# Kernel tuning notes

Hardware: AMD Instinct MI355X
Metric: run time of the kernel (lower is better)

## Reference

```python
import jax, jax.numpy as jnp
import numpy as np

HID, NH, HD = 1024, 16, 64
B, S = 2, 2048


def _gammas(nh):
    # gammas = 1 - exp(linspace(log(1/512), log(1/32), nh))
    lin = np.linspace(np.log(1.0 / 512.0), np.log(1.0 / 32.0), nh)
    return jnp.asarray(1.0 - np.exp(lin), dtype=jnp.float32)


def setup_inputs() -> dict:
    key = jax.random.key(0)
    ks = jax.random.split(key, 6)
    x = jax.random.normal(ks[0], (B, S, HID), dtype=jnp.float32)
    # Per-head retention projection weights (Retention has its own q/k/v of [head_size, head_size])
    wq = jax.random.normal(ks[1], (NH, HD, HD), dtype=jnp.float32) / HD
    wk = jax.random.normal(ks[2], (NH, HD, HD), dtype=jnp.float32) / HD
    wv = jax.random.normal(ks[3], (NH, HD, HD), dtype=jnp.float32) / HD
    w1 = jax.random.normal(ks[4], (HID, HID), dtype=jnp.float32) / HID
    w2 = jax.random.normal(ks[5], (HID, HID), dtype=jnp.float32) / HID
    gn_scale = jnp.ones((HID,), dtype=jnp.float32)
    gn_bias = jnp.zeros((HID,), dtype=jnp.float32)
    return {"x": x, "wq": wq, "wk": wk, "wv": wv, "w1": w1, "w2": w2,
            "gn_scale": gn_scale, "gn_bias": gn_bias}


def reference(x, wq, wk, wv, w1, w2, gn_scale, gn_bias):
    b, s, h = x.shape
    nh, hd = wq.shape[0], wq.shape[1]
    gammas = _gammas(nh)  # [nh]

    xh = x.reshape(b, s, nh, hd)
    q = jnp.einsum('bsnd,nde->bsne', xh, wq)
    k = jnp.einsum('bsnd,nde->bsne', xh, wk)
    v = jnp.einsum('bsnd,nde->bsne', xh, wv)

    # causal decay mask D[n, s, t] = gamma_n ** (s - t) for s >= t else 0
    idx = jnp.arange(s)
    diff = (idx[:, None] - idx[None, :]).astype(jnp.float32)  # [s, s]
    safe = jnp.maximum(diff, 0.0)
    D = jnp.where(diff >= 0,
                  jnp.exp(safe[None] * jnp.log(gammas)[:, None, None]),
                  0.0)  # [nh, s, s]

    scores = jnp.einsum('bsnd,btnd->bnst', q, k) * D[None]      # [b, nh, s, s]
    ret = jnp.einsum('bnst,btnd->bsnd', scores, v)              # [b, s, nh, hd]

    # GroupNorm(num_groups=nh, num_channels=h) over flattened [b*s, h]:
    # normalize within each head-group of hd channels, affine per-channel, eps=1e-5
    mean = ret.mean(axis=-1, keepdims=True)
    var = ret.var(axis=-1, keepdims=True)
    norm = (ret - mean) / jnp.sqrt(var + 1e-5)
    norm = norm.reshape(b, s, h) * gn_scale + gn_bias

    gate = jnp.matmul(x, w1)
    out = gate * jax.nn.sigmoid(gate) + norm  # swish-gated branch + retention
    return jnp.matmul(out, w2)
```

## Files before the change

kernel.cpp:

```cpp
#include <hip/hip_runtime.h>

#define HIDD 1024
#define NHH  16
#define HDD  64
#define BBB  2
#define SSS  2048
#define BS   (BBB * SSS)

typedef __attribute__((ext_vector_type(8))) _Float16 half8;
typedef __attribute__((ext_vector_type(4))) _Float16 half4;
typedef __attribute__((ext_vector_type(4))) float    f32x4;

#define LSCALE 2048.0f
#define LINV   (1.0f / 2048.0f)

static __device__ __forceinline__ f32x4 mfma16h(half8 a, half8 b, f32x4 c) {
    return __builtin_amdgcn_mfma_f32_16x16x32_f16(a, b, c, 0, 0, 0);
}

static __device__ __forceinline__ void split2h(float v, _Float16& h, _Float16& l) {
    h = (_Float16)v;
    l = (_Float16)((v - (float)h) * LSCALE);
}

static __device__ __forceinline__ void gl_lds16(const _Float16* g, _Float16* l) {
    __builtin_amdgcn_global_load_lds(
        (const __attribute__((address_space(1))) unsigned int*)g,
        (__attribute__((address_space(3))) unsigned int*)l,
        16, 0, 0);
}

__global__ __launch_bounds__(256) void k_wprep(const float* __restrict__ wq,
                                               const float* __restrict__ wk,
                                               const float* __restrict__ wv,
                                               _Float16* __restrict__ WTh,
                                               _Float16* __restrict__ WTl) {
    const int blk = blockIdx.x;
    const int mat = blk >> 4, n = blk & 15;
    const float* src = (mat == 0 ? wq : mat == 1 ? wk : wv) + (size_t)n * 4096;
    for (int c = threadIdx.x; c < 4096; c += 256) {
        int e = c >> 6, d = c & 63;
        float v = src[d * 64 + e];
        _Float16 h, l;
        split2h(v, h, l);
        WTh[(size_t)blk * 4096 + c] = h;
        WTl[(size_t)blk * 4096 + c] = l;
    }
}

__global__ __launch_bounds__(512) void k_proj_mfma(const float* __restrict__ x,
                                                   const _Float16* __restrict__ WTh,
                                                   const _Float16* __restrict__ WTl,
                                                   _Float16* __restrict__ Qh, _Float16* __restrict__ Ql,
                                                   _Float16* __restrict__ Kh, _Float16* __restrict__ Kl,
                                                   _Float16* __restrict__ VTh, _Float16* __restrict__ VTl) {
    const int n  = blockIdx.y;
    const int R0 = blockIdx.x * 128;
    const int tid = threadIdx.x;
    const int w = tid >> 6, lane = tid & 63;
    const int hi = lane >> 4, lo = lane & 15;

    __shared__ __align__(16) _Float16 smem[27648];

    half8 ah[2], al[2];
#pragma unroll
    for (int kf = 0; kf < 2; kf++) {
        const float* xp = x + (size_t)(R0 + 16 * w + lo) * HIDD + n * HDD + kf * 32 + 8 * hi;
        float4 v0 = *(const float4*)xp;
        float4 v1 = *(const float4*)(xp + 4);
        float vv[8] = { v0.x, v0.y, v0.z, v0.w, v1.x, v1.y, v1.z, v1.w };
#pragma unroll
        for (int j = 0; j < 8; ++j) {
            _Float16 h, l;
            split2h(vv[j], h, l);
            ah[kf][j] = h; al[kf][j] = l;
        }
    }

    for (int c = tid; c < 3072; c += 512) {
        int m = c >> 10, rest = c & 1023, hl = rest >> 9, cc = rest & 511;
        int r = cc >> 3, j8 = (cc & 7) << 3;
        const _Float16* src = (hl ? WTl : WTh) + ((size_t)(m * NHH + n)) * 4096 + r * 64 + j8;
        *(half8*)&smem[(m * 2 + hl) * 4608 + r * 72 + j8] = *(const half8*)src;
    }
    __syncthreads();

    const int bq = R0 >> 11;
    const int sr = R0 & 2047;
    const size_t bn = (size_t)(bq * NHH + n);
    float vkeep[4][4][2];

    for (int mat = 0; mat < 3; ++mat) {
        const _Float16* bh_base = smem + (mat * 2 + 0) * 4608;
        const _Float16* bl_base = smem + (mat * 2 + 1) * 4608;
        f32x4 a0[4], a1[4];
#pragma unroll
        for (int eb = 0; eb < 4; ++eb) {
            a0[eb] = (f32x4){0.f, 0.f, 0.f, 0.f};
            a1[eb] = (f32x4){0.f, 0.f, 0.f, 0.f};
        }
#pragma unroll
        for (int eb = 0; eb < 4; ++eb) {
            half8 bh0 = *(const half8*)&bh_base[(16 * eb + lo) * 72 + 8 * hi];
            half8 bh1 = *(const half8*)&bh_base[(16 * eb + lo) * 72 + 32 + 8 * hi];
            half8 bl0 = *(const half8*)&bl_base[(16 * eb + lo) * 72 + 8 * hi];
            half8 bl1 = *(const half8*)&bl_base[(16 * eb + lo) * 72 + 32 + 8 * hi];
            a0[eb] = mfma16h(ah[0], bh0, a0[eb]);
            a0[eb] = mfma16h(ah[1], bh1, a0[eb]);
            a1[eb] = mfma16h(ah[0], bl0, a1[eb]);
            a1[eb] = mfma16h(al[0], bh0, a1[eb]);
            a1[eb] = mfma16h(ah[1], bl1, a1[eb]);
            a1[eb] = mfma16h(al[1], bh1, a1[eb]);
        }

        if (mat < 2) {
            _Float16* Dh = (mat == 0) ? Qh : Kh;
            _Float16* Dl = (mat == 0) ? Ql : Kl;
#pragma unroll
            for (int eb = 0; eb < 4; ++eb)
#pragma unroll
                for (int r = 0; r < 4; ++r) {
                    int gr = R0 + 16 * w + 4 * hi + r;
                    int s = gr & 2047;
                    float val = a0[eb][r] + a1[eb][r] * LINV;
                    _Float16 h, l;
                    split2h(val, h, l);
                    size_t idx = (bn * SSS + s) * HDD + 16 * eb + lo;
                    Dh[idx] = h; Dl[idx] = l;
                }
        } else {
#pragma unroll
            for (int eb = 0; eb < 4; ++eb)
#pragma unroll
                for (int r = 0; r < 4; ++r) {
                    vkeep[eb][r][0] = a0[eb][r];
                    vkeep[eb][r][1] = a1[eb][r];
                }
        }
    }

    __syncthreads();
    _Float16* tbh = smem;
    _Float16* tbl = smem + 8704;
#pragma unroll
    for (int eb = 0; eb < 4; ++eb)
#pragma unroll
        for (int r = 0; r < 4; ++r) {
            int rl = 16 * w + 4 * hi + r;
            int ch = 16 * eb + lo;
            _Float16 h, l;
            split2h(vkeep[eb][r][0] + vkeep[eb][r][1] * LINV, h, l);
            tbh[ch * 136 + rl] = h;
            tbl[ch * 136 + rl] = l;
        }
    __syncthreads();
    for (int c = tid; c < 1024; c += 512) {
        int ch = c >> 4, s8 = (c & 15) << 3;
        int a64 = s8 & 64;
        int s0 = s8 & 63;
        int basePerm = a64 + (s0 & 32) + ((s0 >> 3) & 3) * 4;
        const _Float16* th = &tbh[ch * 136];
        const _Float16* tl = &tbl[ch * 136];
        half4 h0 = *(const half4*)(th + basePerm);
        half4 h1 = *(const half4*)(th + basePerm + 16);
        half4 l0 = *(const half4*)(tl + basePerm);
        half4 l1 = *(const half4*)(tl + basePerm + 16);
        half8 oh = {h0[0], h0[1], h0[2], h0[3], h1[0], h1[1], h1[2], h1[3]};
        half8 ol = {l0[0], l0[1], l0[2], l0[3], l1[0], l1[1], l1[2], l1[3]};
        size_t gi = (bn * HDD + ch) * SSS + sr + s8;
        *(half8*)(VTh + gi) = oh;
        *(half8*)(VTl + gi) = ol;
    }
}

__global__ __launch_bounds__(256) void k_ret_mfma(const _Float16* __restrict__ Qh, const _Float16* __restrict__ Ql,
                                                  const _Float16* __restrict__ Kh, const _Float16* __restrict__ Kl,
                                                  const _Float16* __restrict__ VTh, const _Float16* __restrict__ VTl,
                                                  const float* __restrict__ gns,
                                                  const float* __restrict__ gnb,
                                                  float* __restrict__ normb) {
    const int n = blockIdx.y, b = blockIdx.z;
    const int qt = (n < 8) ? ((int)gridDim.x - 1 - (int)blockIdx.x) : (int)blockIdx.x;
    const int tid = threadIdx.x;
    const int w = tid >> 6, lane = tid & 63;
    const int hi = lane >> 4, lo = lane & 15;

    const double l512 = -6.2383246250395075;
    const double l32  = -3.4657359027997265;
    double lin = l512 + (double)n * (l32 - l512) / 15.0;
    float gamma = (float)(1.0 - exp(lin));
    float l2g = log2f(gamma);
    int dmax = (int)(16.0f / (-l2g)) + 1;

    const int qb = qt * 64;
    const int qw = qb + 16 * w;
    int stb_start = (qb > dmax) ? ((qb - dmax) >> 5) : 0;
    const int stb_end  = 2 * qt + 1;
    const int stb_diag = qw >> 5;

    const size_t bn = (size_t)(b * NHH + n);
    const _Float16* Qhp = Qh + bn * SSS * HDD;
    const _Float16* Qlp = Ql + bn * SSS * HDD;
    const _Float16* Khp = Kh + bn * SSS * HDD;
    const _Float16* Klp = Kl + bn * SSS * HDD;
    const _Float16* Vhp = VTh + bn * HDD * SSS;
    const _Float16* Vlp = VTl + bn * HDD * SSS;

    half8 qfh[2], qfl[2];
#pragma unroll
    for (int kf = 0; kf < 2; kf++) {
        size_t o = (size_t)(qw + lo) * HDD + kf * 32 + 8 * hi;
        qfh[kf] = *(const half8*)(Qhp + o);
        qfl[kf] = *(const half8*)(Qlp + o);
    }

    f32x4 acc0[4], acc1[4];
#pragma unroll
    for (int e = 0; e < 4; e++) {
        acc0[e] = (f32x4){0.f, 0.f, 0.f, 0.f};
        acc1[e] = (f32x4){0.f, 0.f, 0.f, 0.f};
    }

    __shared__ __align__(16) _Float16 ksh[4096];
    __shared__ __align__(16) _Float16 ksl[4096];
    __shared__ __align__(16) _Float16 vsh[4096];
    __shared__ __align__(16) _Float16 vsl[4096];

    const _Float16* sg = (w == 0) ? Khp : (w == 1) ? Klp : (w == 2) ? Vhp : Vlp;
    _Float16* slds = (w == 0) ? ksh : (w == 1) ? ksl : (w == 2) ? vsh : vsl;
    size_t goff;
    if (w < 2) goff = (size_t)(lane >> 3) * HDD + (size_t)((((lane & 7) ^ ((lane >> 3) & 7))) << 3);
    else       goff = (size_t)(lane >> 2) * SSS + (size_t)((((lane & 3) ^ ((lane >> 3) & 3))) << 3);

    auto issue = [&](int tbase, int pb) {
        _Float16* Lb = slds + pb * 2048;
        if (w < 2) {
#pragma unroll
            for (int i = 0; i < 4; ++i)
                gl_lds16(sg + (size_t)(tbase + 8 * i) * HDD + goff, Lb + i * 512);
        } else {
#pragma unroll
            for (int i = 0; i < 4; ++i)
                gl_lds16(sg + (size_t)(16 * i) * SSS + tbase + goff, Lb + i * 512);
        }
    };

    const int ks0 = ((hi ^ (lo & 7)) << 3);
    const int ks1 = (((4 + hi) ^ (lo & 7)) << 3);
    const int vs0 = ((hi ^ ((lo >> 1) & 3)) << 3);

    float ftile = exp2f((float)(qw + lo - stb_start * 32) * l2g);
    const float gi16   = exp2f(-16.0f * l2g);
    const float ginv32 = exp2f(-32.0f * l2g);
    float f4[4];
#pragma unroll
    for (int r = 0; r < 4; ++r) f4[r] = exp2f(-(float)(4 * hi + r) * l2g);

    int pb = 0;
    issue(stb_start * 32, 0);
    __syncthreads();

    for (int stb = stb_start; stb <= stb_end; ++stb) {
        const int tbase = stb * 32;
        if (stb < stb_end) issue(tbase + 32, pb ^ 1);

        const bool active = (tbase <= qw + 15) && (tbase + 31 >= qw - dmax);
        if (active) {
            const bool dm = (stb == stb_diag);
            const _Float16* kh_ = &ksh[pb * 2048];
            const _Float16* kl_ = &ksl[pb * 2048];
            const _Float16* vh_ = &vsh[pb * 2048];
            const _Float16* vl_ = &vsl[pb * 2048];
            _Float16 ph4[2][4], pl4[2][4];
#pragma unroll
            for (int tt = 0; tt < 2; ++tt) {
                int rb = (16 * tt + lo) * 64;
                half8 kh0 = *(const half8*)&kh_[rb + ks0];
                half8 kh1 = *(const half8*)&kh_[rb + ks1];
                half8 kl0 = *(const half8*)&kl_[rb + ks0];
                half8 kl1 = *(const half8*)&kl_[rb + ks1];
                f32x4 s0 = (f32x4){0.f, 0.f, 0.f, 0.f};
                f32x4 s1 = (f32x4){0.f, 0.f, 0.f, 0.f};
                s0 = mfma16h(kh0, qfh[0], s0);
                s0 = mfma16h(kh1, qfh[1], s0);
                s1 = mfma16h(kl0, qfh[0], s1);
                s1 = mfma16h(kh0, qfl[0], s1);
                s1 = mfma16h(kl1, qfh[1], s1);
                s1 = mfma16h(kh1, qfl[1], s1);
                const float g = tt ? ftile * gi16 : ftile;
#pragma unroll
                for (int r = 0; r < 4; r++) {
                    float p = (s0[r] + s1[r] * LINV) * (g * f4[r]);
                    if (dm) {
                        int diff = (qw + lo) - (tbase + 16 * tt + 4 * hi + r);
                        if (diff < 0) p = 0.0f;
                    }
                    split2h(p, ph4[tt][r], pl4[tt][r]);
                }
            }
            half8 pfh = (half8){ph4[0][0], ph4[0][1], ph4[0][2], ph4[0][3],
                                ph4[1][0], ph4[1][1], ph4[1][2], ph4[1][3]};
            half8 pfl = (half8){pl4[0][0], pl4[0][1], pl4[0][2], pl4[0][3],
                                pl4[1][0], pl4[1][1], pl4[1][2], pl4[1][3]};
#pragma unroll
            for (int e = 0; e < 4; e++) {
                int vb = (16 * e + lo) * 32 + vs0;
                half8 vh0 = *(const half8*)&vh_[vb];
                half8 vl0 = *(const half8*)&vl_[vb];
                acc0[e] = mfma16h(pfh, vh0, acc0[e]);
                acc1[e] = mfma16h(pfh, vl0, acc1[e]);
                acc1[e] = mfma16h(pfl, vh0, acc1[e]);
            }
        }
        ftile *= ginv32;
        __syncthreads();
        pb ^= 1;
    }

    f32x4 accf[4];
#pragma unroll
    for (int e = 0; e < 4; e++)
#pragma unroll
        for (int r = 0; r < 4; r++)
            accf[e][r] = acc0[e][r] + acc1[e][r] * LINV;

    float s[4], sq[4];
#pragma unroll
    for (int r = 0; r < 4; r++) {
        s[r] = 0.f; sq[r] = 0.f;
#pragma unroll
        for (int e = 0; e < 4; e++) { float v = accf[e][r]; s[r] += v; sq[r] += v * v; }
    }
#pragma unroll
    for (int mask = 1; mask < 16; mask <<= 1)
#pragma unroll
        for (int r = 0; r < 4; r++) {
            s[r]  += __shfl_xor(s[r],  mask);
            sq[r] += __shfl_xor(sq[r], mask);
        }
#pragma unroll
    for (int e = 0; e < 4; e++)
#pragma unroll
        for (int r = 0; r < 4; r++) {
            float mean = s[r] * (1.0f / 64.0f);
            float var  = sq[r] * (1.0f / 64.0f) - mean * mean;
            float rstd = rsqrtf(var + 1e-5f);
            int ch = 16 * e + lo;
            int sg2 = qw + 4 * hi + r;
            float nv = (accf[e][r] - mean) * rstd;
            nv = nv * gns[n * 64 + ch] + gnb[n * 64 + ch];
            normb[((size_t)b * SSS + sg2) * HIDD + n * 64 + ch] = nv;
        }
}

__global__ __launch_bounds__(256) void k_cvt_h(const float* __restrict__ src,
                                               _Float16* __restrict__ dst) {
    int i = blockIdx.x * 256 + threadIdx.x;
    float4 v = reinterpret_cast<const float4*>(src)[i];
    half4 o = { (_Float16)v.x, (_Float16)v.y, (_Float16)v.z, (_Float16)v.w };
    reinterpret_cast<half4*>(dst)[i] = o;
}

__global__ __launch_bounds__(256) void k_tr_h(const float* __restrict__ src,
                                              _Float16* __restrict__ dst,
                                              int K, int N) {
    __shared__ float ls[32][33];
    int kb = blockIdx.y * 32, nb = blockIdx.x * 32;
    int tx = threadIdx.x & 31, ty = threadIdx.x >> 5;
#pragma unroll
    for (int i = 0; i < 4; i++) {
        int r = ty + 8 * i;
        ls[r][tx] = src[(size_t)(kb + r) * N + nb + tx];
    }
    __syncthreads();
#pragma unroll
    for (int i = 0; i < 4; i++) {
        int r = ty + 8 * i;
        dst[(size_t)(nb + r) * K + kb + tx] = (_Float16)ls[tx][r];
    }
}

template <int MODE>
__global__ __launch_bounds__(256) void k_gemm_h(const _Float16* __restrict__ A,
                                                const _Float16* __restrict__ Bt,
                                                const float* __restrict__ normb,
                                                _Float16* __restrict__ Y,
                                                float* __restrict__ Out) {
    const int Rb = blockIdx.x * 128, Cb = blockIdx.y * 128;
    const int tid = threadIdx.x, w = tid >> 6, lane = tid & 63;
    const int hi = lane >> 4, lo = lane & 15;
    const int wm = w >> 1, wn = w & 1;

    __shared__ __align__(16) _Float16 as[128 * 64];
    __shared__ __align__(16) _Float16 bs[128 * 64];

    f32x4 acc[4][4];
#pragma unroll
    for (int m = 0; m < 4; m++)
#pragma unroll
        for (int nn = 0; nn < 4; nn++) acc[m][nn] = (f32x4){0.f, 0.f, 0.f, 0.f};

    const _Float16* gM = (w < 2) ? (A + (size_t)(Rb + 64 * (w & 1)) * HIDD)
                                 : (Bt + (size_t)(Cb + 64 * (w & 1)) * HIDD);
    _Float16* gL = ((w < 2) ? as : bs) + (w & 1) * 64 * 64;
    const size_t gofs = (size_t)(lane >> 3) * HIDD
                      + (size_t)((((lane & 7) ^ ((lane >> 3) & 7))) << 3);

    int rsw[2];
#pragma unroll
    for (int kf = 0; kf < 2; kf++) rsw[kf] = ((4 * kf + hi) ^ (lo & 7)) << 3;

    for (int kk = 0; kk < 16; ++kk) {
        __syncthreads();
#pragma unroll
        for (int i = 0; i < 8; ++i)
            gl_lds16(gM + (size_t)(8 * i) * HIDD + kk * 64 + gofs, gL + i * 512);
        __syncthreads();

        half8 af[4][2], bf[4][2];
#pragma unroll
        for (int m = 0; m < 4; m++) {
            int row = 64 * wm + 16 * m + lo;
#pragma unroll
            for (int kf = 0; kf < 2; kf++)
                af[m][kf] = *(const half8*)&as[row * 64 + rsw[kf]];
        }
#pragma unroll
        for (int nn = 0; nn < 4; nn++) {
            int row = 64 * wn + 16 * nn + lo;
#pragma unroll
            for (int kf = 0; kf < 2; kf++)
                bf[nn][kf] = *(const half8*)&bs[row * 64 + rsw[kf]];
        }
#pragma unroll
        for (int m = 0; m < 4; m++)
#pragma unroll
            for (int nn = 0; nn < 4; nn++) {
                acc[m][nn] = mfma16h(af[m][0], bf[nn][0], acc[m][nn]);
                acc[m][nn] = mfma16h(af[m][1], bf[nn][1], acc[m][nn]);
            }
    }

#pragma unroll
    for (int m = 0; m < 4; m++)
#pragma unroll
        for (int nn = 0; nn < 4; nn++)
#pragma unroll
            for (int r = 0; r < 4; r++) {
                int row = Rb + 64 * wm + 16 * m + 4 * hi + r;
                int col = Cb + 64 * wn + 16 * nn + lo;
                float v = acc[m][nn][r];
                size_t idx = (size_t)row * HIDD + col;
                if (MODE == 0) {
                    float sw = v / (1.0f + expf(-v));
                    float y = sw + normb[idx];
                    Y[idx] = (_Float16)y;
                } else {
                    Out[idx] = v;
                }
            }
}

extern "C" void kernel_launch(void* const* d_in, const int* in_sizes, int n_in,
                              void* d_out, int out_size, void* d_ws, size_t ws_size,
                              hipStream_t stream) {
    const float* x   = (const float*)d_in[0];
    const float* wq  = (const float*)d_in[1];
    const float* wk  = (const float*)d_in[2];
    const float* wv  = (const float*)d_in[3];
    const float* w1  = (const float*)d_in[4];
    const float* w2  = (const float*)d_in[5];
    const float* gns = (const float*)d_in[6];
    const float* gnb = (const float*)d_in[7];
    float* out = (float*)d_out;

    char* base = (char*)d_ws;
    size_t off = 0;
    auto carve = [&](size_t bytes) -> void* {
        void* p = base + off;
        off += (bytes + 255) & ~(size_t)255;
        return p;
    };
    _Float16* Qh  = (_Float16*)carve((size_t)BS * HIDD * 2);
    _Float16* Ql  = (_Float16*)carve((size_t)BS * HIDD * 2);
    _Float16* Kh  = (_Float16*)carve((size_t)BS * HIDD * 2);
    _Float16* Kl  = (_Float16*)carve((size_t)BS * HIDD * 2);
    _Float16* VTh = (_Float16*)carve((size_t)BS * HIDD * 2);
    _Float16* VTl = (_Float16*)carve((size_t)BS * HIDD * 2);
    float*    normb = (float*)carve((size_t)BS * HIDD * 4);
    _Float16* WTh = (_Float16*)normb;
    _Float16* WTl = WTh + (size_t)48 * 4096;
    _Float16* xh  = Qh;
    _Float16* w1t = Kh;
    _Float16* w2t = Kh + (size_t)HIDD * HIDD;
    _Float16* yh  = VTh;
    (void)ws_size; (void)in_sizes; (void)n_in; (void)out_size;

    k_wprep<<<48, 256, 0, stream>>>(wq, wk, wv, WTh, WTl);
    k_proj_mfma<<<dim3(BS / 128, NHH), 512, 0, stream>>>(x, WTh, WTl,
                                                         Qh, Ql, Kh, Kl, VTh, VTl);
    k_ret_mfma<<<dim3(SSS / 64, NHH, BBB), 256, 0, stream>>>(Qh, Ql, Kh, Kl, VTh, VTl,
                                                             gns, gnb, normb);
    k_cvt_h<<<(BS * HIDD) / 4 / 256, 256, 0, stream>>>(x, xh);
    k_tr_h<<<dim3(32, 32), 256, 0, stream>>>(w1, w1t, HIDD, HIDD);
    k_tr_h<<<dim3(32, 32), 256, 0, stream>>>(w2, w2t, HIDD, HIDD);
    k_gemm_h<0><<<dim3(BS / 128, HIDD / 128), 256, 0, stream>>>(xh, w1t, normb, yh, nullptr);
    k_gemm_h<1><<<dim3(BS / 128, HIDD / 128), 256, 0, stream>>>(yh, w2t, nullptr, nullptr, out);
}
```

Baseline: 166.1 us.

## Make retention kernel persistent with atomic work queue; double-buffer GEMM LDS loads

Turns the retention kernel into a persistent kernel of 512 blocks that pull (query tile, head, batch) work items from a global atomic counter, heaviest query tiles first, to balance the triangular causal workload across CUs. The counter lives in the output buffer and is zeroed with a memset before launch; the later GEMM overwrites that buffer. Separately, the FP16 GEMM now double-buffers its LDS tiles so the next K slice loads while the current one is multiplied, with one barrier per iteration instead of two. The trade-offs are doubled GEMM LDS use, which may lower occupancy, plus atomic and barrier overhead per work item.

```diff
diff --git a/kernel.cpp b/kernel.cpp
--- a/kernel.cpp
+++ b/kernel.cpp
@@ -178,179 +178,193 @@
                                                   const _Float16* __restrict__ VTh, const _Float16* __restrict__ VTl,
                                                   const float* __restrict__ gns,
                                                   const float* __restrict__ gnb,
-                                                  float* __restrict__ normb) {
-    const int n = blockIdx.y, b = blockIdx.z;
-    const int qt = (n < 8) ? ((int)gridDim.x - 1 - (int)blockIdx.x) : (int)blockIdx.x;
+                                                  float* __restrict__ normb,
+                                                  unsigned* __restrict__ counter) {
     const int tid = threadIdx.x;
     const int w = tid >> 6, lane = tid & 63;
     const int hi = lane >> 4, lo = lane & 15;
-
-    const double l512 = -6.2383246250395075;
-    const double l32  = -3.4657359027997265;
-    double lin = l512 + (double)n * (l32 - l512) / 15.0;
-    float gamma = (float)(1.0 - exp(lin));
-    float l2g = log2f(gamma);
-    int dmax = (int)(16.0f / (-l2g)) + 1;
-
-    const int qb = qt * 64;
-    const int qw = qb + 16 * w;
-    int stb_start = (qb > dmax) ? ((qb - dmax) >> 5) : 0;
-    const int stb_end  = 2 * qt + 1;
-    const int stb_diag = qw >> 5;
-
-    const size_t bn = (size_t)(b * NHH + n);
-    const _Float16* Qhp = Qh + bn * SSS * HDD;
-    const _Float16* Qlp = Ql + bn * SSS * HDD;
-    const _Float16* Khp = Kh + bn * SSS * HDD;
-    const _Float16* Klp = Kl + bn * SSS * HDD;
-    const _Float16* Vhp = VTh + bn * HDD * SSS;
-    const _Float16* Vlp = VTl + bn * HDD * SSS;
-
-    half8 qfh[2], qfl[2];
-#pragma unroll
-    for (int kf = 0; kf < 2; kf++) {
-        size_t o = (size_t)(qw + lo) * HDD + kf * 32 + 8 * hi;
-        qfh[kf] = *(const half8*)(Qhp + o);
-        qfl[kf] = *(const half8*)(Qlp + o);
-    }
-
-    f32x4 acc0[4], acc1[4];
-#pragma unroll
-    for (int e = 0; e < 4; e++) {
-        acc0[e] = (f32x4){0.f, 0.f, 0.f, 0.f};
-        acc1[e] = (f32x4){0.f, 0.f, 0.f, 0.f};
-    }
 
     __shared__ __align__(16) _Float16 ksh[4096];
     __shared__ __align__(16) _Float16 ksl[4096];
     __shared__ __align__(16) _Float16 vsh[4096];
     __shared__ __align__(16) _Float16 vsl[4096];
-
-    const _Float16* sg = (w == 0) ? Khp : (w == 1) ? Klp : (w == 2) ? Vhp : Vlp;
-    _Float16* slds = (w == 0) ? ksh : (w == 1) ? ksl : (w == 2) ? vsh : vsl;
-    size_t goff;
-    if (w < 2) goff = (size_t)(lane >> 3) * HDD + (size_t)((((lane & 7) ^ ((lane >> 3) & 7))) << 3);
-    else       goff = (size_t)(lane >> 2) * SSS + (size_t)((((lane & 3) ^ ((lane >> 3) & 3))) << 3);
-
-    auto issue = [&](int tbase, int pb) {
-        _Float16* Lb = slds + pb * 2048;
-        if (w < 2) {
-#pragma unroll
-            for (int i = 0; i < 4; ++i)
-                gl_lds16(sg + (size_t)(tbase + 8 * i) * HDD + goff, Lb + i * 512);
-        } else {
-#pragma unroll
-            for (int i = 0; i < 4; ++i)
-                gl_lds16(sg + (size_t)(16 * i) * SSS + tbase + goff, Lb + i * 512);
-        }
-    };
+    __shared__ unsigned sitem;
 
     const int ks0 = ((hi ^ (lo & 7)) << 3);
     const int ks1 = (((4 + hi) ^ (lo & 7)) << 3);
     const int vs0 = ((hi ^ ((lo >> 1) & 3)) << 3);
-
-    float ftile = exp2f((float)(qw + lo - stb_start * 32) * l2g);
-    const float gi16   = exp2f(-16.0f * l2g);
-    const float ginv32 = exp2f(-32.0f * l2g);
-    float f4[4];
-#pragma unroll
-    for (int r = 0; r < 4; ++r) f4[r] = exp2f(-(float)(4 * hi + r) * l2g);
-
-    int pb = 0;
-    issue(stb_start * 32, 0);
-    __syncthreads();
-
-    for (int stb = stb_start; stb <= stb_end; ++stb) {
-        const int tbase = stb * 32;
-        if (stb < stb_end) issue(tbase + 32, pb ^ 1);
-
-        const bool active = (tbase <= qw + 15) && (tbase + 31 >= qw - dmax);
-        if (active) {
-            const bool dm = (stb == stb_diag);
-            const _Float16* kh_ = &ksh[pb * 2048];
-            const _Float16* kl_ = &ksl[pb * 2048];
-            const _Float16* vh_ = &vsh[pb * 2048];
-            const _Float16* vl_ = &vsl[pb * 2048];
-            _Float16 ph4[2][4], pl4[2][4];
-#pragma unroll
-            for (int tt = 0; tt < 2; ++tt) {
-                int rb = (16 * tt + lo) * 64;
-                half8 kh0 = *(const half8*)&kh_[rb + ks0];
-                half8 kh1 = *(const half8*)&kh_[rb + ks1];
-                half8 kl0 = *(const half8*)&kl_[rb + ks0];
-                half8 kl1 = *(const half8*)&kl_[rb + ks1];
-                f32x4 s0 = (f32x4){0.f, 0.f, 0.f, 0.f};
-                f32x4 s1 = (f32x4){0.f, 0.f, 0.f, 0.f};
-                s0 = mfma16h(kh0, qfh[0], s0);
-                s0 = mfma16h(kh1, qfh[1], s0);
-                s1 = mfma16h(kl0, qfh[0], s1);
-                s1 = mfma16h(kh0, qfl[0], s1);
-                s1 = mfma16h(kl1, qfh[1], s1);
-                s1 = mfma16h(kh1, qfl[1], s1);
-                const float g = tt ? ftile * gi16 : ftile;
-#pragma unroll
-                for (int r = 0; r < 4; r++) {
-                    float p = (s0[r] + s1[r] * LINV) * (g * f4[r]);
-                    if (dm) {
-                        int diff = (qw + lo) - (tbase + 16 * tt + 4 * hi + r);
-                        if (diff < 0) p = 0.0f;
+    size_t goffK = (size_t)(lane >> 3) * HDD + (size_t)((((lane & 7) ^ ((lane >> 3) & 7))) << 3);
+    size_t goffV = (size_t)(lane >> 2) * SSS + (size_t)((((lane & 3) ^ ((lane >> 3) & 3))) << 3);
+
+    const double l512 = -6.2383246250395075;
+    const double l32  = -3.4657359027997265;
+
+    while (true) {
+        if (tid == 0) sitem = atomicAdd(counter, 1u);
+        __syncthreads();
+        const unsigned it = sitem;
+        __syncthreads();
+        if (it >= 1024u) break;
+
+        const int qt = 31 - (int)(it >> 5);
+        const int n  = (int)(it & 15);
+        const int b  = (int)((it >> 4) & 1);
+
+        double lin = l512 + (double)n * (l32 - l512) / 15.0;
+        float gamma = (float)(1.0 - exp(lin));
+        float l2g = log2f(gamma);
+        int dmax = (int)(16.0f / (-l2g)) + 1;
+
+        const int qb = qt * 64;
+        const int qw = qb + 16 * w;
+        int stb_start = (qb > dmax) ? ((qb - dmax) >> 5) : 0;
+        const int stb_end  = 2 * qt + 1;
+        const int stb_diag = qw >> 5;
+
+        const size_t bn = (size_t)(b * NHH + n);
+        const _Float16* Qhp = Qh + bn * SSS * HDD;
+        const _Float16* Qlp = Ql + bn * SSS * HDD;
+        const _Float16* Khp = Kh + bn * SSS * HDD;
+        const _Float16* Klp = Kl + bn * SSS * HDD;
+        const _Float16* Vhp = VTh + bn * HDD * SSS;
+        const _Float16* Vlp = VTl + bn * HDD * SSS;
+
+        half8 qfh[2], qfl[2];
+#pragma unroll
+        for (int kf = 0; kf < 2; kf++) {
+            size_t o = (size_t)(qw + lo) * HDD + kf * 32 + 8 * hi;
+            qfh[kf] = *(const half8*)(Qhp + o);
+            qfl[kf] = *(const half8*)(Qlp + o);
+        }
+
+        f32x4 acc0[4], acc1[4];
+#pragma unroll
+        for (int e = 0; e < 4; e++) {
+            acc0[e] = (f32x4){0.f, 0.f, 0.f, 0.f};
+            acc1[e] = (f32x4){0.f, 0.f, 0.f, 0.f};
+        }
+
+        const _Float16* sg = (w == 0) ? Khp : (w == 1) ? Klp : (w == 2) ? Vhp : Vlp;
+        _Float16* slds = (w == 0) ? ksh : (w == 1) ? ksl : (w == 2) ? vsh : vsl;
+        const size_t goff = (w < 2) ? goffK : goffV;
+
+        auto issue = [&](int tbase, int pbuf) {
+            _Float16* Lb = slds + pbuf * 2048;
+            if (w < 2) {
+#pragma unroll
+                for (int i = 0; i < 4; ++i)
+                    gl_lds16(sg + (size_t)(tbase + 8 * i) * HDD + goff, Lb + i * 512);
+            } else {
+#pragma unroll
+                for (int i = 0; i < 4; ++i)
+                    gl_lds16(sg + (size_t)(16 * i) * SSS + tbase + goff, Lb + i * 512);
+            }
+        };
+
+        float ftile = exp2f((float)(qw + lo - stb_start * 32) * l2g);
+        const float gi16   = exp2f(-16.0f * l2g);
+        const float ginv32 = exp2f(-32.0f * l2g);
+        float f4[4];
+#pragma unroll
+        for (int r = 0; r < 4; ++r) f4[r] = exp2f(-(float)(4 * hi + r) * l2g);
+
+        int pb = 0;
+        issue(stb_start * 32, 0);
+        __syncthreads();
+
+        for (int stb = stb_start; stb <= stb_end; ++stb) {
+            const int tbase = stb * 32;
+            if (stb < stb_end) issue(tbase + 32, pb ^ 1);
+
+            const bool active = (tbase <= qw + 15) && (tbase + 31 >= qw - dmax);
+            if (active) {
+                const bool dm = (stb == stb_diag);
+                const _Float16* kh_ = &ksh[pb * 2048];
+                const _Float16* kl_ = &ksl[pb * 2048];
+                const _Float16* vh_ = &vsh[pb * 2048];
+                const _Float16* vl_ = &vsl[pb * 2048];
+                _Float16 ph4[2][4], pl4[2][4];
+#pragma unroll
+                for (int tt = 0; tt < 2; ++tt) {
+                    int rb = (16 * tt + lo) * 64;
+                    half8 kh0 = *(const half8*)&kh_[rb + ks0];
+                    half8 kh1 = *(const half8*)&kh_[rb + ks1];
+                    half8 kl0 = *(const half8*)&kl_[rb + ks0];
+                    half8 kl1 = *(const half8*)&kl_[rb + ks1];
+                    f32x4 s0 = (f32x4){0.f, 0.f, 0.f, 0.f};
+                    f32x4 s1 = (f32x4){0.f, 0.f, 0.f, 0.f};
+                    s0 = mfma16h(kh0, qfh[0], s0);
+                    s0 = mfma16h(kh1, qfh[1], s0);
+                    s1 = mfma16h(kl0, qfh[0], s1);
+                    s1 = mfma16h(kh0, qfl[0], s1);
+                    s1 = mfma16h(kl1, qfh[1], s1);
+                    s1 = mfma16h(kh1, qfl[1], s1);
+                    const float g = tt ? ftile * gi16 : ftile;
+#pragma unroll
+                    for (int r = 0; r < 4; r++) {
+                        float p = (s0[r] + s1[r] * LINV) * (g * f4[r]);
+                        if (dm) {
+                            int diff = (qw + lo) - (tbase + 16 * tt + 4 * hi + r);
+                            if (diff < 0) p = 0.0f;
+                        }
+                        split2h(p, ph4[tt][r], pl4[tt][r]);
                     }
-                    split2h(p, ph4[tt][r], pl4[tt][r]);
+                }
+                half8 pfh = (half8){ph4[0][0], ph4[0][1], ph4[0][2], ph4[0][3],
+                                    ph4[1][0], ph4[1][1], ph4[1][2], ph4[1][3]};
+                half8 pfl = (half8){pl4[0][0], pl4[0][1], pl4[0][2], pl4[0][3],
+                                    pl4[1][0], pl4[1][1], pl4[1][2], pl4[1][3]};
+#pragma unroll
+                for (int e = 0; e < 4; e++) {
+                    int vb = (16 * e + lo) * 32 + vs0;
+                    half8 vh0 = *(const half8*)&vh_[vb];
+                    half8 vl0 = *(const half8*)&vl_[vb];
+                    acc0[e] = mfma16h(pfh, vh0, acc0[e]);
+                    acc1[e] = mfma16h(pfh, vl0, acc1[e]);
+                    acc1[e] = mfma16h(pfl, vh0, acc1[e]);
                 }
             }
-            half8 pfh = (half8){ph4[0][0], ph4[0][1], ph4[0][2], ph4[0][3],
-                                ph4[1][0], ph4[1][1], ph4[1][2], ph4[1][3]};
-            half8 pfl = (half8){pl4[0][0], pl4[0][1], pl4[0][2], pl4[0][3],
-                                pl4[1][0], pl4[1][1], pl4[1][2], pl4[1][3]};
-#pragma unroll
-            for (int e = 0; e < 4; e++) {
-                int vb = (16 * e + lo) * 32 + vs0;
-                half8 vh0 = *(const half8*)&vh_[vb];
-                half8 vl0 = *(const half8*)&vl_[vb];
-                acc0[e] = mfma16h(pfh, vh0, acc0[e]);
-                acc1[e] = mfma16h(pfh, vl0, acc1[e]);
-                acc1[e] = mfma16h(pfl, vh0, acc1[e]);
+            ftile *= ginv32;
+            __syncthreads();
+            pb ^= 1;
+        }
+
+        f32x4 accf[4];
+#pragma unroll
+        for (int e = 0; e < 4; e++)
+#pragma unroll
+            for (int r = 0; r < 4; r++)
+                accf[e][r] = acc0[e][r] + acc1[e][r] * LINV;
+
+        float s[4], sq[4];
+#pragma unroll
+        for (int r = 0; r < 4; r++) {
+            s[r] = 0.f; sq[r] = 0.f;
+#pragma unroll
+            for (int e = 0; e < 4; e++) { float v = accf[e][r]; s[r] += v; sq[r] += v * v; }
+        }
+#pragma unroll
+        for (int mask = 1; mask < 16; mask <<= 1)
+#pragma unroll
+            for (int r = 0; r < 4; r++) {
+                s[r]  += __shfl_xor(s[r],  mask);
+                sq[r] += __shfl_xor(sq[r], mask);
             }
-        }
-        ftile *= ginv32;
+#pragma unroll
+        for (int e = 0; e < 4; e++)
+#pragma unroll
+            for (int r = 0; r < 4; r++) {
+                float mean = s[r] * (1.0f / 64.0f);
+                float var  = sq[r] * (1.0f / 64.0f) - mean * mean;
+                float rstd = rsqrtf(var + 1e-5f);
+                int ch = 16 * e + lo;
+                int sg2 = qw + 4 * hi + r;
+                float nv = (accf[e][r] - mean) * rstd;
+                nv = nv * gns[n * 64 + ch] + gnb[n * 64 + ch];
+                normb[((size_t)b * SSS + sg2) * HIDD + n * 64 + ch] = nv;
+            }
         __syncthreads();
-        pb ^= 1;
-    }
-
-    f32x4 accf[4];
-#pragma unroll
-    for (int e = 0; e < 4; e++)
-#pragma unroll
-        for (int r = 0; r < 4; r++)
-            accf[e][r] = acc0[e][r] + acc1[e][r] * LINV;
-
-    float s[4], sq[4];
-#pragma unroll
-    for (int r = 0; r < 4; r++) {
-        s[r] = 0.f; sq[r] = 0.f;
-#pragma unroll
-        for (int e = 0; e < 4; e++) { float v = accf[e][r]; s[r] += v; sq[r] += v * v; }
-    }
-#pragma unroll
-    for (int mask = 1; mask < 16; mask <<= 1)
-#pragma unroll
-        for (int r = 0; r < 4; r++) {
-            s[r]  += __shfl_xor(s[r],  mask);
-            sq[r] += __shfl_xor(sq[r], mask);
-        }
-#pragma unroll
-    for (int e = 0; e < 4; e++)
-#pragma unroll
-        for (int r = 0; r < 4; r++) {
-            float mean = s[r] * (1.0f / 64.0f);
-            float var  = sq[r] * (1.0f / 64.0f) - mean * mean;
-            float rstd = rsqrtf(var + 1e-5f);
-            int ch = 16 * e + lo;
-            int sg2 = qw + 4 * hi + r;
-            float nv = (accf[e][r] - mean) * rstd;
-            nv = nv * gns[n * 64 + ch] + gnb[n * 64 + ch];
-            normb[((size_t)b * SSS + sg2) * HIDD + n * 64 + ch] = nv;
-        }
+    }
 }
 
 __global__ __launch_bounds__(256) void k_cvt_h(const float* __restrict__ src,
@@ -391,8 +405,8 @@
     const int hi = lane >> 4, lo = lane & 15;
     const int wm = w >> 1, wn = w & 1;
 
-    __shared__ __align__(16) _Float16 as[128 * 64];
-    __shared__ __align__(16) _Float16 bs[128 * 64];
+    __shared__ __align__(16) _Float16 as[2][128 * 64];
+    __shared__ __align__(16) _Float16 bs[2][128 * 64];
 
     f32x4 acc[4][4];
 #pragma unroll
@@ -402,20 +416,27 @@
 
     const _Float16* gM = (w < 2) ? (A + (size_t)(Rb + 64 * (w & 1)) * HIDD)
                                  : (Bt + (size_t)(Cb + 64 * (w & 1)) * HIDD);
-    _Float16* gL = ((w < 2) ? as : bs) + (w & 1) * 64 * 64;
+    const int wsel = (w < 2) ? 0 : 1;
     const size_t gofs = (size_t)(lane >> 3) * HIDD
                       + (size_t)((((lane & 7) ^ ((lane >> 3) & 7))) << 3);
 
-    int rsw[2];
-#pragma unroll
-    for (int kf = 0; kf < 2; kf++) rsw[kf] = ((4 * kf + hi) ^ (lo & 7)) << 3;
-
-    for (int kk = 0; kk < 16; ++kk) {
-        __syncthreads();
+    auto issue = [&](int kk, int pbuf) {
+        _Float16* gL = (wsel ? bs[pbuf] : as[pbuf]) + (w & 1) * 64 * 64;
 #pragma unroll
         for (int i = 0; i < 8; ++i)
             gl_lds16(gM + (size_t)(8 * i) * HIDD + kk * 64 + gofs, gL + i * 512);
-        __syncthreads();
+    };
+
+    int rsw[2];
+#pragma unroll
+    for (int kf = 0; kf < 2; kf++) rsw[kf] = ((4 * kf + hi) ^ (lo & 7)) << 3;
+
+    int pb = 0;
+    issue(0, 0);
+    __syncthreads();
+
+    for (int kk = 0; kk < 16; ++kk) {
+        if (kk < 15) issue(kk + 1, pb ^ 1);
 
         half8 af[4][2], bf[4][2];
 #pragma unroll
@@ -423,14 +444,14 @@
             int row = 64 * wm + 16 * m + lo;
 #pragma unroll
             for (int kf = 0; kf < 2; kf++)
-                af[m][kf] = *(const half8*)&as[row * 64 + rsw[kf]];
+                af[m][kf] = *(const half8*)&as[pb][row * 64 + rsw[kf]];
         }
 #pragma unroll
         for (int nn = 0; nn < 4; nn++) {
             int row = 64 * wn + 16 * nn + lo;
 #pragma unroll
             for (int kf = 0; kf < 2; kf++)
-                bf[nn][kf] = *(const half8*)&bs[row * 64 + rsw[kf]];
+                bf[nn][kf] = *(const half8*)&bs[pb][row * 64 + rsw[kf]];
         }
 #pragma unroll
         for (int m = 0; m < 4; m++)
@@ -439,6 +460,8 @@
                 acc[m][nn] = mfma16h(af[m][0], bf[nn][0], acc[m][nn]);
                 acc[m][nn] = mfma16h(af[m][1], bf[nn][1], acc[m][nn]);
             }
+        __syncthreads();
+        pb ^= 1;
     }
 
 #pragma unroll
@@ -494,13 +517,15 @@
     _Float16* w1t = Kh;
     _Float16* w2t = Kh + (size_t)HIDD * HIDD;
     _Float16* yh  = VTh;
+    unsigned* counter = (unsigned*)d_out;
     (void)ws_size; (void)in_sizes; (void)n_in; (void)out_size;
 
     k_wprep<<<48, 256, 0, stream>>>(wq, wk, wv, WTh, WTl);
     k_proj_mfma<<<dim3(BS / 128, NHH), 512, 0, stream>>>(x, WTh, WTl,
                                                          Qh, Ql, Kh, Kl, VTh, VTl);
-    k_ret_mfma<<<dim3(SSS / 64, NHH, BBB), 256, 0, stream>>>(Qh, Ql, Kh, Kl, VTh, VTl,
-                                                             gns, gnb, normb);
+    hipMemsetAsync(counter, 0, sizeof(unsigned), stream);
+    k_ret_mfma<<<512, 256, 0, stream>>>(Qh, Ql, Kh, Kl, VTh, VTl,
+                                        gns, gnb, normb, counter);
     k_cvt_h<<<(BS * HIDD) / 4 / 256, 256, 0, stream>>>(x, xh);
     k_tr_h<<<dim3(32, 32), 256, 0, stream>>>(w1, w1t, HIDD, HIDD);
     k_tr_h<<<dim3(32, 32), 256, 0, stream>>>(w2, w2t, HIDD, HIDD);
```

Result: faster. 145.9 us (-12.2%).
